# Performance work log

Measured on AMD Instinct MI355X. Metric: run time of the kernel, lower is better.

The kernel has to match this reference:

```python
import jax, jax.numpy as jnp
import numpy as np

B, S, D, E, K, F = 2, 1024, 1024, 8, 2, 2048


def setup_inputs() -> dict:
    key = jax.random.key(0)
    k0, k1, k2, k3 = jax.random.split(key, 4)
    x = jax.random.normal(k0, (B, S, D), dtype=jnp.float32)
    gate_w = (jax.random.normal(k1, (E, D), dtype=jnp.float32) * 0.02)  # nn.init.normal_(std=0.02)
    # nn.Linear default init ~ U(-1/sqrt(fan_in), 1/sqrt(fan_in)); use same scale
    w1 = jax.random.uniform(k2, (E, F, D), dtype=jnp.float32, minval=-1.0, maxval=1.0) / np.float32(np.sqrt(D))
    w2 = jax.random.uniform(k3, (E, D, F), dtype=jnp.float32, minval=-1.0, maxval=1.0) / np.float32(np.sqrt(F))
    norm_w = jnp.ones((D,), dtype=jnp.float32)
    scale = jnp.full((1,), -4.0, dtype=jnp.float32)
    return {"x": x, "gate_w": gate_w, "w1": w1, "w2": w2, "norm_w": norm_w, "scale": scale}


def reference(x, gate_w, w1, w2, norm_w, scale):
    b, s, d = x.shape
    e = gate_w.shape[0]
    t = b * s
    eps = jnp.finfo(x.dtype).eps  # torch RMSNorm eps=None -> dtype eps
    # RMSNorm
    xn = x * jax.lax.rsqrt(jnp.mean(x * x, axis=-1, keepdims=True) + eps) * norm_w
    xf = xn.reshape(t, d)
    # router
    logits = xf @ gate_w.T                       # [T, E]
    prob = jax.nn.softmax(logits, axis=-1)
    topk_w, topk_e = jax.lax.top_k(prob, K)      # [T, K]
    topk_w = topk_w / jnp.clip(jnp.sum(topk_w, axis=-1, keepdims=True), 1e-6)
    # dense combine weights [T, E]: sum of slot weights routed to each expert
    combine = jnp.sum(jax.nn.one_hot(topk_e, e, dtype=xf.dtype) * topk_w[..., None], axis=1)
    # all-expert FFN, weighted combine (same math as the gather/index_add loop)
    h = jax.nn.silu(jnp.einsum('td,efd->tef', xf, w1))   # [T, E, F]
    out = jnp.einsum('tef,edf,te->td', h, w2, combine)    # [T, D]
    # load-balance aux loss (Switch eq.4), f_e from top-1 slot, detached
    f_e = jnp.mean(jax.nn.one_hot(topk_e[:, 0], e, dtype=prob.dtype), axis=0)
    lb_loss = e * jnp.sum(jax.lax.stop_gradient(f_e) * jnp.mean(prob, axis=0))
    sc = jax.nn.sigmoid(scale)[0]
    return (x + sc * out.reshape(b, s, d), lb_loss)
```

## Files before the change

### kernel.cpp

```cpp
#include <hip/hip_runtime.h>
#include <stdint.h>

#define T_TOK 2048
#define DD 1024
#define EE 8
#define FF 2048
#define NSLOT 4096
#define SLOTPAD 4224

typedef __attribute__((ext_vector_type(8))) __bf16 bf16x8;
typedef __attribute__((ext_vector_type(4))) float floatx4;
typedef __attribute__((ext_vector_type(8))) float floatx8;
typedef __attribute__((ext_vector_type(8))) unsigned short ushort8;

__device__ __forceinline__ unsigned short f2bf(float f){
  union { float f; unsigned u; } v; v.f = f;
  unsigned r = v.u + 0x7fffu + ((v.u >> 16) & 1u);
  return (unsigned short)(r >> 16);
}
__device__ __forceinline__ float bf2f(unsigned short h){
  union { unsigned u; float f; } v; v.u = (unsigned)h << 16; return v.f;
}

#define GLDS(src, dst) __builtin_amdgcn_global_load_lds( \
    (__attribute__((address_space(1))) unsigned int*)(src), \
    (__attribute__((address_space(3))) unsigned int*)(dst), 16, 0, 0)

__global__ __launch_bounds__(256) void k_rms_router(
    const float* __restrict__ x, const float* __restrict__ gw,
    const float* __restrict__ nw,
    unsigned short* __restrict__ xn,
    int* __restrict__ topk_id, float* __restrict__ topk_w,
    float* __restrict__ probbuf)
{
  const int t = blockIdx.x, tid = threadIdx.x;
  const float4 xv = ((const float4*)(x + (size_t)t * DD))[tid];
  float ss = xv.x*xv.x + xv.y*xv.y + xv.z*xv.z + xv.w*xv.w;
  #pragma unroll
  for (int o = 32; o > 0; o >>= 1) ss += __shfl_down(ss, o);
  __shared__ float s_ss[4];
  __shared__ float s_p[4][8];
  if ((tid & 63) == 0) s_ss[tid >> 6] = ss;
  __syncthreads();
  const float tot = s_ss[0] + s_ss[1] + s_ss[2] + s_ss[3];
  const float inv = rsqrtf(tot * (1.0f / DD) + 1.1920929e-7f);
  const float4 nv = ((const float4*)nw)[tid];
  float4 xnv;
  xnv.x = xv.x*inv*nv.x; xnv.y = xv.y*inv*nv.y;
  xnv.z = xv.z*inv*nv.z; xnv.w = xv.w*inv*nv.w;
  ushort4 bv; bv.x = f2bf(xnv.x); bv.y = f2bf(xnv.y); bv.z = f2bf(xnv.z); bv.w = f2bf(xnv.w);
  ((ushort4*)(xn + (size_t)t * DD))[tid] = bv;
  float p[8];
  #pragma unroll
  for (int e = 0; e < 8; e++){
    const float4 g = ((const float4*)(gw + e * DD))[tid];
    p[e] = xnv.x*g.x + xnv.y*g.y + xnv.z*g.z + xnv.w*g.w;
  }
  #pragma unroll
  for (int e = 0; e < 8; e++){
    #pragma unroll
    for (int o = 32; o > 0; o >>= 1) p[e] += __shfl_down(p[e], o);
  }
  if ((tid & 63) == 0){
    #pragma unroll
    for (int e = 0; e < 8; e++) s_p[tid >> 6][e] = p[e];
  }
  __syncthreads();
  if (tid == 0){
    float lg[8], pr[8];
    #pragma unroll
    for (int e = 0; e < 8; e++) lg[e] = s_p[0][e] + s_p[1][e] + s_p[2][e] + s_p[3][e];
    float mx = lg[0];
    for (int e = 1; e < 8; e++) mx = fmaxf(mx, lg[e]);
    float sum = 0.f;
    for (int e = 0; e < 8; e++){ pr[e] = __expf(lg[e] - mx); sum += pr[e]; }
    const float is = 1.f / sum;
    for (int e = 0; e < 8; e++) pr[e] *= is;
    #pragma unroll
    for (int e = 0; e < 8; e++) probbuf[t * 8 + e] = pr[e];
    int e1 = 0;
    for (int e = 1; e < 8; e++) if (pr[e] > pr[e1]) e1 = e;
    int e2 = (e1 == 0) ? 1 : 0;
    for (int e = 0; e < 8; e++) if (e != e1 && e != e2 && pr[e] > pr[e2]) e2 = e;
    const float wsum = fmaxf(pr[e1] + pr[e2], 1e-6f);
    topk_id[2*t] = e1; topk_id[2*t+1] = e2;
    topk_w[2*t] = pr[e1] / wsum; topk_w[2*t+1] = pr[e2] / wsum;
  }
}

__global__ __launch_bounds__(256) void k_stats(
    const int* __restrict__ topk_id, const float* __restrict__ topk_w,
    const float* __restrict__ probbuf,
    int* __restrict__ counts, int* __restrict__ bases,
    int* __restrict__ slots_of, int* __restrict__ tok_of,
    float* __restrict__ slot_w,
    float* __restrict__ lb_out)
{
  const int tid = threadIdx.x;
  __shared__ int s_scan[256][8];
  __shared__ int s_base[8];

  int ids[16];
  int lc[8] = {}, lc1[8] = {};
  float lsp[8] = {};
  #pragma unroll
  for (int j = 0; j < 8; j++){
    const int t = tid * 8 + j;
    const int e1 = topk_id[2*t], e2 = topk_id[2*t+1];
    ids[2*j] = e1; ids[2*j+1] = e2;
    lc[e1]++; lc[e2]++; lc1[e1]++;
    const float4 p0 = ((const float4*)(probbuf + t * 8))[0];
    const float4 p1 = ((const float4*)(probbuf + t * 8))[1];
    lsp[0] += p0.x; lsp[1] += p0.y; lsp[2] += p0.z; lsp[3] += p0.w;
    lsp[4] += p1.x; lsp[5] += p1.y; lsp[6] += p1.z; lsp[7] += p1.w;
  }
  #pragma unroll
  for (int e = 0; e < 8; e++) s_scan[tid][e] = lc[e];
  __syncthreads();
  for (int off = 1; off < 256; off <<= 1){
    int v[8];
    if (tid >= off){
      #pragma unroll
      for (int e = 0; e < 8; e++) v[e] = s_scan[tid - off][e];
    }
    __syncthreads();
    if (tid >= off){
      #pragma unroll
      for (int e = 0; e < 8; e++) s_scan[tid][e] += v[e];
    }
    __syncthreads();
  }
  int   rc1[8]; float rsp[8];
  #pragma unroll
  for (int e = 0; e < 8; e++){ rc1[e] = lc1[e]; rsp[e] = lsp[e]; }
  #pragma unroll
  for (int e = 0; e < 8; e++){
    #pragma unroll
    for (int o = 32; o > 0; o >>= 1){
      rc1[e] += __shfl_down(rc1[e], o);
      rsp[e] += __shfl_down(rsp[e], o);
    }
  }
  __shared__ int   s_c1[4][8];
  __shared__ float s_sp[4][8];
  if ((tid & 63) == 0){
    const int w = tid >> 6;
    #pragma unroll
    for (int e = 0; e < 8; e++){ s_c1[w][e] = rc1[e]; s_sp[w][e] = rsp[e]; }
  }
  __syncthreads();
  if (tid == 0){
    int b = 0; float lb = 0.f;
    for (int e = 0; e < 8; e++){
      const int tot = s_scan[255][e];
      counts[e] = tot; bases[e] = b; s_base[e] = b; b += tot;
      const int   c1 = s_c1[0][e] + s_c1[1][e] + s_c1[2][e] + s_c1[3][e];
      const float sp = s_sp[0][e] + s_sp[1][e] + s_sp[2][e] + s_sp[3][e];
      lb += (float)c1 * sp;
    }
    lb_out[0] = 8.f * lb * (1.f / ((float)T_TOK * (float)T_TOK));
  }
  __syncthreads();
  int rank[8];
  #pragma unroll
  for (int e = 0; e < 8; e++) rank[e] = s_scan[tid][e] - lc[e];
  #pragma unroll
  for (int j = 0; j < 8; j++){
    const int t = tid * 8 + j;
    #pragma unroll
    for (int k = 0; k < 2; k++){
      const int e = ids[2*j + k];
      const int slot = s_base[e] + rank[e]++;
      slots_of[2*t + k] = slot;
      tok_of[slot] = t;
      slot_w[slot] = topk_w[2*t + k];
    }
  }
}

template<int KD, int NDIM, int MODE>
__global__ __launch_bounds__(256, 3) void k_gemm(
    const unsigned short* __restrict__ Ag,
    const float* __restrict__ Bw,
    const int* __restrict__ counts, const int* __restrict__ bases,
    const int* __restrict__ tok_of,
    unsigned short* __restrict__ Cout)
{
  const int e = blockIdx.x & 7;
  const int g = blockIdx.x >> 3;
  int nt, ms, kbase; size_t poff;
  if (MODE == 0){ nt = g & 31; ms = g >> 5; kbase = 0; poff = 0; }
  else { const int ks = g & 1; nt = (g >> 1) & 15; ms = g >> 5; kbase = ks * 1024;
         poff = (size_t)ks * SLOTPAD * NDIM; }
  const int M = counts[e];
  if (M == 0) return;
  const int sbase = bases[e];

  __shared__ __align__(16) unsigned short As[3][128 * 32];
  __shared__ __align__(16) float          Bsf[3][64 * 32];

  const int tid = threadIdx.x;
  const int l = tid & 63;
  const int w = tid >> 6;
  const int wm = (w >> 1) * 64, wn = (w & 1) * 32;
  const int lrow = l & 15, lq = l >> 4;

  const int ar0 = tid >> 2, ar1 = (tid + 256) >> 2, aq = tid & 3;
  const int akc0 = ((aq - (ar0 >> 1)) & 3) * 8;
  const int akc1 = ((aq - (ar1 >> 1)) & 3) * 8;
  const int br0 = tid >> 3;
  const int bq  = tid & 7;
  const int bkc = ((bq - br0) & 7) * 4;

  const float* bsrc0 = Bw + (size_t)e * NDIM * KD + (size_t)(nt * 64 + br0) * KD + kbase + bkc;
  const float* bsrc1 = bsrc0 + (size_t)32 * KD;

#define STAGE_TILE(SLOT, KO) do { \
      GLDS(arow0 + (KO), As[SLOT] + tid * 8); \
      GLDS(arow1 + (KO), As[SLOT] + (tid + 256) * 8); \
      GLDS(bsrc0 + (KO), Bsf[SLOT] + tid * 4); \
      GLDS(bsrc1 + (KO), Bsf[SLOT] + (tid + 256) * 4); \
    } while (0)

#define KSTEP(CB) do { \
      bf16x8 af[4], bfv[2]; \
      _Pragma("unroll") \
      for (int mi = 0; mi < 4; mi++){ \
        const int row = wm + mi * 16 + lrow; \
        const int p = (lq + (row >> 1)) & 3; \
        af[mi] = *(const bf16x8*)(As[CB] + row * 32 + p * 8); \
      } \
      _Pragma("unroll") \
      for (int ni = 0; ni < 2; ni++){ \
        const int row = wn + ni * 16 + lrow; \
        const int pp0 = (2 * lq + row) & 7; \
        const int pp1 = (2 * lq + 1 + row) & 7; \
        const float4 u0 = *(const float4*)(Bsf[CB] + row * 32 + pp0 * 4); \
        const float4 u1 = *(const float4*)(Bsf[CB] + row * 32 + pp1 * 4); \
        floatx8 uf; \
        uf[0]=u0.x; uf[1]=u0.y; uf[2]=u0.z; uf[3]=u0.w; \
        uf[4]=u1.x; uf[5]=u1.y; uf[6]=u1.z; uf[7]=u1.w; \
        bfv[ni] = __builtin_convertvector(uf, bf16x8); \
      } \
      _Pragma("unroll") \
      for (int mi = 0; mi < 4; mi++) \
        _Pragma("unroll") \
        for (int ni = 0; ni < 2; ni++) \
          acc[mi][ni] = __builtin_amdgcn_mfma_f32_16x16x32_bf16(af[mi], bfv[ni], acc[mi][ni], 0, 0, 0); \
    } while (0)

  for (int mt = ms; mt * 128 < M; mt += 4){
    const unsigned short *arow0, *arow1;
    {
      const int v0 = min(mt * 128 + ar0, M - 1);
      const int v1 = min(mt * 128 + ar1, M - 1);
      const int r0 = (MODE == 0) ? tok_of[sbase + v0] : (sbase + v0);
      const int r1 = (MODE == 0) ? tok_of[sbase + v1] : (sbase + v1);
      arow0 = Ag + (size_t)r0 * KD + kbase + akc0;
      arow1 = Ag + (size_t)r1 * KD + kbase + akc1;
    }

    floatx4 acc[4][2] = {};

    STAGE_TILE(0, 0);
    STAGE_TILE(1, 32);

    #pragma unroll 3
    for (int kt = 0; kt < 30; kt++){
      asm volatile("s_waitcnt vmcnt(4)" ::: "memory");
      __builtin_amdgcn_sched_barrier(0);
      __builtin_amdgcn_s_barrier();
      __builtin_amdgcn_sched_barrier(0);
      const int cur = kt % 3;
      const int s2 = (kt + 2) % 3;
      STAGE_TILE(s2, (kt + 2) * 32);
      KSTEP(cur);
    }
    asm volatile("s_waitcnt vmcnt(4)" ::: "memory");
    __builtin_amdgcn_sched_barrier(0);
    __builtin_amdgcn_s_barrier();
    __builtin_amdgcn_sched_barrier(0);
    KSTEP(0);
    asm volatile("s_waitcnt vmcnt(0)" ::: "memory");
    __builtin_amdgcn_sched_barrier(0);
    __builtin_amdgcn_s_barrier();
    __builtin_amdgcn_sched_barrier(0);
    KSTEP(1);

    const int rb = lq * 4;
    #pragma unroll
    for (int mi = 0; mi < 4; mi++){
      #pragma unroll
      for (int r = 0; r < 4; r++){
        const int row = mt * 128 + wm + mi * 16 + rb + r;
        if (row < M){
          #pragma unroll
          for (int ni = 0; ni < 2; ni++){
            const int col = nt * 64 + wn + ni * 16 + lrow;
            const float v = acc[mi][ni][r];
            if (MODE == 0){
              const float s = v / (1.f + __expf(-v));
              Cout[(size_t)(sbase + row) * NDIM + col] = f2bf(s);
            } else {
              Cout[poff + (size_t)(sbase + row) * NDIM + col] = f2bf(v);
            }
          }
        }
      }
    }
    __syncthreads();
  }
#undef STAGE_TILE
#undef KSTEP
}

__global__ __launch_bounds__(256) void k_combine(
    const float* __restrict__ x, const unsigned short* __restrict__ Og,
    const int* __restrict__ slots_of, const float* __restrict__ slot_w,
    const float* __restrict__ scale,
    float* __restrict__ out)
{
  const int i = blockIdx.x * 256 + threadIdx.x;
  const int t = i >> 7;
  const int j = i & 127;
  const int s0 = slots_of[2*t], s1 = slots_of[2*t+1];
  const float w0 = slot_w[s0], w1 = slot_w[s1];
  const ushort8 a0 = ((const ushort8*)(Og + (size_t)s0 * DD))[j];
  const ushort8 a1 = ((const ushort8*)(Og + (size_t)SLOTPAD * DD + (size_t)s0 * DD))[j];
  const ushort8 b0 = ((const ushort8*)(Og + (size_t)s1 * DD))[j];
  const ushort8 b1 = ((const ushort8*)(Og + (size_t)SLOTPAD * DD + (size_t)s1 * DD))[j];
  const float4 x0 = ((const float4*)(x + (size_t)t * DD))[2*j];
  const float4 x1 = ((const float4*)(x + (size_t)t * DD))[2*j + 1];
  const float sc = 1.f / (1.f + __expf(-scale[0]));
  float o[8];
  #pragma unroll
  for (int q = 0; q < 8; q++)
    o[q] = sc * (w0 * (bf2f(a0[q]) + bf2f(a1[q])) + w1 * (bf2f(b0[q]) + bf2f(b1[q])));
  float4 o0, o1;
  o0.x = x0.x + o[0]; o0.y = x0.y + o[1]; o0.z = x0.z + o[2]; o0.w = x0.w + o[3];
  o1.x = x1.x + o[4]; o1.y = x1.y + o[5]; o1.z = x1.z + o[6]; o1.w = x1.w + o[7];
  ((float4*)(out + (size_t)t * DD))[2*j] = o0;
  ((float4*)(out + (size_t)t * DD))[2*j + 1] = o1;
}

extern "C" void kernel_launch(void* const* d_in, const int* in_sizes, int n_in,
                              void* d_out, int out_size, void* d_ws, size_t ws_size,
                              hipStream_t stream)
{
  const float* x     = (const float*)d_in[0];
  const float* gw    = (const float*)d_in[1];
  const float* w1    = (const float*)d_in[2];
  const float* w2    = (const float*)d_in[3];
  const float* nw    = (const float*)d_in[4];
  const float* scale = (const float*)d_in[5];
  float* out = (float*)d_out;

  char* ws = (char*)d_ws;
  int*   counts  = (int*)(ws + 0);
  int*   bases   = (int*)(ws + 64);
  int*   topk_id = (int*)(ws + 1024);
  float* topk_w  = (float*)(ws + 20480);
  int*   slots_of= (int*)(ws + 40960);
  float* slot_w  = (float*)(ws + 61440);
  int*   tok_of  = (int*)(ws + 81920);
  float* probbuf = (float*)(ws + 102400);
  unsigned short* xn  = (unsigned short*)(ws + 262144);
  unsigned short* Hg  = xn + (size_t)T_TOK * DD;
  unsigned short* Og  = Hg + (size_t)SLOTPAD * FF;

  k_rms_router<<<T_TOK, 256, 0, stream>>>(x, gw, nw, xn, topk_id, topk_w, probbuf);
  k_stats<<<1, 256, 0, stream>>>(topk_id, topk_w, probbuf, counts, bases,
                                 slots_of, tok_of, slot_w, out + (size_t)T_TOK * DD);
  k_gemm<1024, 2048, 0><<<EE * 4 * 32, 256, 0, stream>>>(xn, w1, counts, bases, tok_of, Hg);
  k_gemm<2048, 1024, 1><<<EE * 4 * 16 * 2, 256, 0, stream>>>(Hg, w2, counts, bases, nullptr, Og);
  k_combine<<<T_TOK * DD / 8 / 256, 256, 0, stream>>>(x, Og, slots_of, slot_w, scale, out);
}
```

Baseline: 262.9 us.

## Flatten grouped GEMM into per-tile grid using prefix-summed expert tile offsets

The stats kernel now computes a prefix sum of 128-row tile counts per expert. Both grouped GEMMs launch a flat grid in which each block maps to one (expert, m-tile, n/k-split) tile, found by searching that prefix. Previously each expert got a fixed slice of 4 m-strided blocks that looped over tiles. The goal is to balance load when expert sizes are skewed and to drop the per-block loop. The fixed grid of 1280 assumes at most 40 tiles in total, which holds because 4096 slots across 8 experts give at most 39 tiles. Surplus blocks exit early.

```diff
diff --git a/kernel.cpp b/kernel.cpp
--- a/kernel.cpp
+++ b/kernel.cpp
@@ -7,6 +7,7 @@
 #define FF 2048
 #define NSLOT 4096
 #define SLOTPAD 4224
+#define GEMM_GRID 1280
 
 typedef __attribute__((ext_vector_type(8))) __bf16 bf16x8;
 typedef __attribute__((ext_vector_type(4))) float floatx4;
@@ -92,6 +93,7 @@
     const int* __restrict__ topk_id, const float* __restrict__ topk_w,
     const float* __restrict__ probbuf,
     int* __restrict__ counts, int* __restrict__ bases,
+    int* __restrict__ tile_base,
     int* __restrict__ slots_of, int* __restrict__ tok_of,
     float* __restrict__ slot_w,
     float* __restrict__ lb_out)
@@ -150,14 +152,16 @@
   }
   __syncthreads();
   if (tid == 0){
-    int b = 0; float lb = 0.f;
+    int b = 0; float lb = 0.f; int tb = 0;
     for (int e = 0; e < 8; e++){
       const int tot = s_scan[255][e];
       counts[e] = tot; bases[e] = b; s_base[e] = b; b += tot;
+      tile_base[e] = tb; tb += (tot + 127) >> 7;
       const int   c1 = s_c1[0][e] + s_c1[1][e] + s_c1[2][e] + s_c1[3][e];
       const float sp = s_sp[0][e] + s_sp[1][e] + s_sp[2][e] + s_sp[3][e];
       lb += (float)c1 * sp;
     }
+    tile_base[8] = tb;
     lb_out[0] = 8.f * lb * (1.f / ((float)T_TOK * (float)T_TOK));
   }
   __syncthreads();
@@ -183,17 +187,23 @@
     const unsigned short* __restrict__ Ag,
     const float* __restrict__ Bw,
     const int* __restrict__ counts, const int* __restrict__ bases,
+    const int* __restrict__ tile_base,
     const int* __restrict__ tok_of,
     unsigned short* __restrict__ Cout)
 {
-  const int e = blockIdx.x & 7;
-  const int g = blockIdx.x >> 3;
-  int nt, ms, kbase; size_t poff;
-  if (MODE == 0){ nt = g & 31; ms = g >> 5; kbase = 0; poff = 0; }
-  else { const int ks = g & 1; nt = (g >> 1) & 15; ms = g >> 5; kbase = ks * 1024;
+  const int tile = blockIdx.x;
+  if (tile >= tile_base[8] * 32) return;
+  int e = 0;
+  #pragma unroll
+  for (int i = 0; i < 7; i++) e += (tile >= tile_base[i + 1] * 32) ? 1 : 0;
+  const int local = tile - tile_base[e] * 32;
+  const int mt = local >> 5;
+  const int q  = local & 31;
+  int nt, kbase; size_t poff;
+  if (MODE == 0){ nt = q; kbase = 0; poff = 0; }
+  else { nt = q & 15; const int ks = q >> 4; kbase = ks * 1024;
          poff = (size_t)ks * SLOTPAD * NDIM; }
   const int M = counts[e];
-  if (M == 0) return;
   const int sbase = bases[e];
 
   __shared__ __align__(16) unsigned short As[3][128 * 32];
@@ -214,6 +224,16 @@
 
   const float* bsrc0 = Bw + (size_t)e * NDIM * KD + (size_t)(nt * 64 + br0) * KD + kbase + bkc;
   const float* bsrc1 = bsrc0 + (size_t)32 * KD;
+
+  const unsigned short *arow0, *arow1;
+  {
+    const int v0 = min(mt * 128 + ar0, M - 1);
+    const int v1 = min(mt * 128 + ar1, M - 1);
+    const int r0 = (MODE == 0) ? tok_of[sbase + v0] : (sbase + v0);
+    const int r1 = (MODE == 0) ? tok_of[sbase + v1] : (sbase + v1);
+    arow0 = Ag + (size_t)r0 * KD + kbase + akc0;
+    arow1 = Ag + (size_t)r1 * KD + kbase + akc1;
+  }
 
 #define STAGE_TILE(SLOT, KO) do { \
       GLDS(arow0 + (KO), As[SLOT] + tid * 8); \
@@ -249,66 +269,53 @@
           acc[mi][ni] = __builtin_amdgcn_mfma_f32_16x16x32_bf16(af[mi], bfv[ni], acc[mi][ni], 0, 0, 0); \
     } while (0)
 
-  for (int mt = ms; mt * 128 < M; mt += 4){
-    const unsigned short *arow0, *arow1;
-    {
-      const int v0 = min(mt * 128 + ar0, M - 1);
-      const int v1 = min(mt * 128 + ar1, M - 1);
-      const int r0 = (MODE == 0) ? tok_of[sbase + v0] : (sbase + v0);
-      const int r1 = (MODE == 0) ? tok_of[sbase + v1] : (sbase + v1);
-      arow0 = Ag + (size_t)r0 * KD + kbase + akc0;
-      arow1 = Ag + (size_t)r1 * KD + kbase + akc1;
-    }
-
-    floatx4 acc[4][2] = {};
-
-    STAGE_TILE(0, 0);
-    STAGE_TILE(1, 32);
-
-    #pragma unroll 3
-    for (int kt = 0; kt < 30; kt++){
-      asm volatile("s_waitcnt vmcnt(4)" ::: "memory");
-      __builtin_amdgcn_sched_barrier(0);
-      __builtin_amdgcn_s_barrier();
-      __builtin_amdgcn_sched_barrier(0);
-      const int cur = kt % 3;
-      const int s2 = (kt + 2) % 3;
-      STAGE_TILE(s2, (kt + 2) * 32);
-      KSTEP(cur);
-    }
+  floatx4 acc[4][2] = {};
+
+  STAGE_TILE(0, 0);
+  STAGE_TILE(1, 32);
+
+  #pragma unroll 3
+  for (int kt = 0; kt < 30; kt++){
     asm volatile("s_waitcnt vmcnt(4)" ::: "memory");
     __builtin_amdgcn_sched_barrier(0);
     __builtin_amdgcn_s_barrier();
     __builtin_amdgcn_sched_barrier(0);
-    KSTEP(0);
-    asm volatile("s_waitcnt vmcnt(0)" ::: "memory");
-    __builtin_amdgcn_sched_barrier(0);
-    __builtin_amdgcn_s_barrier();
-    __builtin_amdgcn_sched_barrier(0);
-    KSTEP(1);
-
-    const int rb = lq * 4;
-    #pragma unroll
-    for (int mi = 0; mi < 4; mi++){
-      #pragma unroll
-      for (int r = 0; r < 4; r++){
-        const int row = mt * 128 + wm + mi * 16 + rb + r;
-        if (row < M){
-          #pragma unroll
-          for (int ni = 0; ni < 2; ni++){
-            const int col = nt * 64 + wn + ni * 16 + lrow;
-            const float v = acc[mi][ni][r];
-            if (MODE == 0){
-              const float s = v / (1.f + __expf(-v));
-              Cout[(size_t)(sbase + row) * NDIM + col] = f2bf(s);
-            } else {
-              Cout[poff + (size_t)(sbase + row) * NDIM + col] = f2bf(v);
-            }
+    const int cur = kt % 3;
+    const int s2 = (kt + 2) % 3;
+    STAGE_TILE(s2, (kt + 2) * 32);
+    KSTEP(cur);
+  }
+  asm volatile("s_waitcnt vmcnt(4)" ::: "memory");
+  __builtin_amdgcn_sched_barrier(0);
+  __builtin_amdgcn_s_barrier();
+  __builtin_amdgcn_sched_barrier(0);
+  KSTEP(0);
+  asm volatile("s_waitcnt vmcnt(0)" ::: "memory");
+  __builtin_amdgcn_sched_barrier(0);
+  __builtin_amdgcn_s_barrier();
+  __builtin_amdgcn_sched_barrier(0);
+  KSTEP(1);
+
+  const int rb = lq * 4;
+  #pragma unroll
+  for (int mi = 0; mi < 4; mi++){
+    #pragma unroll
+    for (int r = 0; r < 4; r++){
+      const int row = mt * 128 + wm + mi * 16 + rb + r;
+      if (row < M){
+        #pragma unroll
+        for (int ni = 0; ni < 2; ni++){
+          const int col = nt * 64 + wn + ni * 16 + lrow;
+          const float v = acc[mi][ni][r];
+          if (MODE == 0){
+            const float s2v = v / (1.f + __expf(-v));
+            Cout[(size_t)(sbase + row) * NDIM + col] = f2bf(s2v);
+          } else {
+            Cout[poff + (size_t)(sbase + row) * NDIM + col] = f2bf(v);
           }
         }
       }
     }
-    __syncthreads();
   }
 #undef STAGE_TILE
 #undef KSTEP
@@ -358,6 +365,7 @@
   char* ws = (char*)d_ws;
   int*   counts  = (int*)(ws + 0);
   int*   bases   = (int*)(ws + 64);
+  int*   tilebase= (int*)(ws + 128);
   int*   topk_id = (int*)(ws + 1024);
   float* topk_w  = (float*)(ws + 20480);
   int*   slots_of= (int*)(ws + 40960);
@@ -369,9 +377,9 @@
   unsigned short* Og  = Hg + (size_t)SLOTPAD * FF;
 
   k_rms_router<<<T_TOK, 256, 0, stream>>>(x, gw, nw, xn, topk_id, topk_w, probbuf);
-  k_stats<<<1, 256, 0, stream>>>(topk_id, topk_w, probbuf, counts, bases,
+  k_stats<<<1, 256, 0, stream>>>(topk_id, topk_w, probbuf, counts, bases, tilebase,
                                  slots_of, tok_of, slot_w, out + (size_t)T_TOK * DD);
-  k_gemm<1024, 2048, 0><<<EE * 4 * 32, 256, 0, stream>>>(xn, w1, counts, bases, tok_of, Hg);
-  k_gemm<2048, 1024, 1><<<EE * 4 * 16 * 2, 256, 0, stream>>>(Hg, w2, counts, bases, nullptr, Og);
+  k_gemm<1024, 2048, 0><<<GEMM_GRID, 256, 0, stream>>>(xn, w1, counts, bases, tilebase, tok_of, Hg);
+  k_gemm<2048, 1024, 1><<<GEMM_GRID, 256, 0, stream>>>(Hg, w2, counts, bases, tilebase, nullptr, Og);
   k_combine<<<T_TOK * DD / 8 / 256, 256, 0, stream>>>(x, Og, slots_of, slot_w, scale, out);
 }
```

After: 281.6 us. 1.07x slower.
